# Kernel tuning notes

Measured on AMD Instinct MI355X. Metric: run time of the kernel, lower is better.

Reference implementation:

```python
import jax, jax.numpy as jnp
import numpy as np

B, V, M, L, D, OUT = 16, 16, 32, 24, 128, 193
VOCAB = {'cond': 5000, 'proc': 2000, 'drug': 600, 'lab_item': 700, 'lab_value': 200, 'inj_item': 400, 'inj_value': 200}


def setup_inputs() -> dict:
    key = jax.random.key(0)
    ks = iter(jax.random.split(key, 48))
    def emb_table(v):
        t = 0.02 * jax.random.normal(next(ks), (v, D), jnp.float32)
        return t.at[0].set(0.0)  # padding_idx = 0
    inp = {}
    inp['tok_cond'] = jax.random.randint(next(ks), (B, V, L), 0, VOCAB['cond'])
    inp['tok_proc'] = jax.random.randint(next(ks), (B, V, L), 0, VOCAB['proc'])
    inp['tok_drug'] = jax.random.randint(next(ks), (B, V, L), 0, VOCAB['drug'])
    inp['tok_lab_item'] = jax.random.randint(next(ks), (B, V, M, L), 0, VOCAB['lab_item'])
    inp['tok_lab_value'] = jax.random.randint(next(ks), (B, V, M, L), 0, VOCAB['lab_value'])
    inp['tok_inj_item'] = jax.random.randint(next(ks), (B, V, M, L), 0, VOCAB['inj_item'])
    inp['tok_inj_value'] = jax.random.randint(next(ks), (B, V, M, L), 0, VOCAB['inj_value'])
    inp['weight'] = jax.random.uniform(next(ks), (B, V, 1), jnp.float32)
    inp['age'] = jax.random.uniform(next(ks), (B, V, 1), jnp.float32)
    for n in ['cond', 'proc', 'drug', 'lab_item', 'lab_value', 'inj_item', 'inj_value']:
        inp['emb_' + n] = emb_table(VOCAB[n])
    def gru_params(nk):
        s = 0.05
        return (s * jax.random.normal(next(ks), (nk, 3 * D, D), jnp.float32),
                s * jax.random.normal(next(ks), (nk, 3 * D, D), jnp.float32),
                jnp.zeros((nk, 3 * D), jnp.float32),
                jnp.zeros((nk, 3 * D), jnp.float32))
    inp['mgru_wih'], inp['mgru_whh'], inp['mgru_bih'], inp['mgru_bhh'] = gru_params(5)
    inp['vgru_wih'], inp['vgru_whh'], inp['vgru_bih'], inp['vgru_bhh'] = gru_params(7)
    inp['info_w'] = 0.05 * jax.random.normal(next(ks), (2, D), jnp.float32)  # Linear(1, D) weights for weight/age
    inp['info_b'] = jnp.zeros((2, D), jnp.float32)
    inp['fc_w'] = 0.05 * jax.random.normal(next(ks), (7 * D, OUT), jnp.float32)
    inp['fc_b'] = jnp.zeros((OUT,), jnp.float32)
    return inp


def _gru(x, wih, whh, bih, bhh):
    # x: [N, T, Din]; torch nn.GRU semantics, gate order (r, z, n), h0 = 0
    n_, t_, _ = x.shape
    d = whh.shape[1]
    xg = jnp.einsum('ntd,gd->ntg', x, wih) + bih  # precompute input gates [N, T, 3D]
    def step(h, xg_t):
        gh = h @ whh.T + bhh
        ir, iz, inn = jnp.split(xg_t, 3, axis=-1)
        hr, hz, hn = jnp.split(gh, 3, axis=-1)
        r = jax.nn.sigmoid(ir + hr)
        z = jax.nn.sigmoid(iz + hz)
        n = jnp.tanh(inn + r * hn)
        h2 = (1.0 - z) * n + z * h
        return h2, h2
    h0 = jnp.zeros((n_, d), x.dtype)
    hT, outs = jax.lax.scan(step, h0, jnp.swapaxes(xg, 0, 1))
    return jnp.swapaxes(outs, 0, 1), hT  # output [N,T,D], hidden [N,D]

_gru_keys = jax.vmap(_gru)  # vmap over the per-feature-key leading axis


def reference(tok_cond, tok_proc, tok_drug, tok_lab_item, tok_lab_value, tok_inj_item, tok_inj_value,
              weight, age, emb_cond, emb_proc, emb_drug, emb_lab_item, emb_lab_value, emb_inj_item,
              emb_inj_value, mgru_wih, mgru_whh, mgru_bih, mgru_bhh, vgru_wih, vgru_whh, vgru_bih,
              vgru_bhh, info_w, info_b, fc_w, fc_b):
    b, v, m, _ = tok_lab_item.shape
    d = emb_cond.shape[1]
    # visit-event features: embedding + sum over code dim (dropout = identity, eval mode)
    e_cond = emb_cond[tok_cond].sum(axis=2)  # [B,V,D]
    e_proc = emb_proc[tok_proc].sum(axis=2)
    e_drug = emb_drug[tok_drug].sum(axis=2)
    # monitor-event pairs: elementwise mul of the two embeddings, sum over code dim
    lab = (emb_lab_item[tok_lab_item] * emb_lab_value[tok_lab_value]).sum(axis=3)  # [B,V,M,D]
    inj = (emb_inj_item[tok_inj_item] * emb_inj_value[tok_inj_value]).sum(axis=3)
    # repeat visit embeddings across the monitor axis (repeat(1, max_monitors, 1))
    rep = lambda e: jnp.broadcast_to(e[:, :, None, :], (b, v, m, d))
    mon_in = jnp.stack([rep(e_cond), rep(e_proc), rep(e_drug), lab, inj], axis=0)
    mon_in = mon_in.reshape(5, b * v, m, d)  # aggregate_tensors with uniform lengths
    # per-key monitor-level GRUs
    mon_out, mon_h = _gru_keys(mon_in, mgru_wih, mgru_whh, mgru_bih, mgru_bhh)
    # split_tensor + extract_and_transpose: take last monitor step per visit -> [5,B,V,D]
    last = mon_out[:, :, -1, :].reshape(5, b, v, d)
    # patient info Linear(1, D) for weight / age
    w_emb = weight * info_w[0] + info_b[0]  # [B,V,D]
    a_emb = age * info_w[1] + info_b[1]
    vis_in = jnp.concatenate([last, jnp.stack([w_emb, a_emb], axis=0)], axis=0)  # [7,B,V,D]
    # per-key visit-level GRUs
    _, vis_h = _gru_keys(vis_in, vgru_wih, vgru_whh, vgru_bih, vgru_bhh)  # [7,B,D]
    patient_emb = jnp.transpose(vis_h, (1, 0, 2)).reshape(b, 7 * d)  # concatenate_patient_embeddings
    logits = jax.nn.relu(patient_emb) @ fc_w + fc_b  # fc_patient: ReLU -> Linear(7D, output_size)
    return logits
```

## Files before the change

### kernel.cpp

```cpp
#include <hip/hip_runtime.h>
#include <stdint.h>

typedef unsigned short u16;
typedef unsigned int u32;

#define B_ 16
#define V_ 16
#define M_ 32
#define L_ 24
#define D_ 128
#define G_ 384
#define N_ 256
#define NM_ 8192
#define OUT_ 193

using bf16x8 = __attribute__((ext_vector_type(8))) __bf16;
using floatx4 = __attribute__((ext_vector_type(4))) float;

__device__ __forceinline__ float bf2f(u16 u) {
  u32 x = ((u32)u) << 16;
  return __builtin_bit_cast(float, x);
}
__device__ __forceinline__ u16 f2bf(float f) {
  u32 u = __builtin_bit_cast(u32, f);
  u = (u + 0x7FFFu + ((u >> 16) & 1u)) >> 16;
  return (u16)u;
}
__device__ __forceinline__ float sigm_(float x) {
  return __builtin_amdgcn_rcpf(1.0f + __expf(-x));
}
__device__ __forceinline__ float tanh_(float x) {
  float e = __expf(2.0f * x);
  return 1.0f - 2.0f * __builtin_amdgcn_rcpf(e + 1.0f);
}
__device__ __forceinline__ floatx4 mfma16(bf16x8 a, bf16x8 b, floatx4 c) {
  return __builtin_amdgcn_mfma_f32_16x16x32_bf16(a, b, c, 0, 0, 0);
}
__device__ __forceinline__ void lds_barrier() {
  asm volatile("s_waitcnt lgkmcnt(0)\n\ts_barrier" ::: "memory");
}

#define CONVB 4608
#define VEB 128
#define PEB 4096

__global__ __launch_bounds__(256) void k_stage1(
    const int* __restrict__ tc, const int* __restrict__ tp, const int* __restrict__ td,
    const int* __restrict__ tli, const int* __restrict__ tlv,
    const int* __restrict__ tii, const int* __restrict__ tiv,
    const float* __restrict__ ec, const float* __restrict__ ep, const float* __restrict__ ed,
    const float* __restrict__ eli, const float* __restrict__ elv,
    const float* __restrict__ eii, const float* __restrict__ eiv,
    const float* __restrict__ wv, const float* __restrict__ av,
    const float* __restrict__ iw, const float* __restrict__ ib,
    const float* __restrict__ mwih, const float* __restrict__ vwih,
    const float* __restrict__ mwhh, const float* __restrict__ vwhh,
    u16* __restrict__ wih_hi, u16* __restrict__ whh_hi,
    u16* __restrict__ ce_hi, u16* __restrict__ ce_lo,
    u16* __restrict__ vx_hi, u16* __restrict__ vx_lo,
    u16* __restrict__ mx_hi, u16* __restrict__ mx_lo) {
  int blk = blockIdx.x, tid = threadIdx.x;
  if (blk < CONVB) {
    const int SW = 12 * G_ * D_, S5 = 5 * G_ * D_;
    int i = blk * 256 + tid;
    if (i < SW) {
      float v = (i < S5) ? mwih[i] : vwih[i - S5];
      wih_hi[i] = f2bf(v);
    } else {
      int o = i - SW;
      float v = (o < S5) ? mwhh[o] : vwhh[o - S5];
      whh_hi[o] = f2bf(v);
    }
  } else if (blk < CONVB + VEB) {
    int n = (blk - CONVB) * 2 + (tid >> 7);
    int d = tid & 127;
    float a0 = 0.f, a1 = 0.f, a2 = 0.f;
#pragma unroll 4
    for (int l = 0; l < L_; l++) {
      a0 += ec[(size_t)tc[n * L_ + l] * D_ + d];
      a1 += ep[(size_t)tp[n * L_ + l] * D_ + d];
      a2 += ed[(size_t)td[n * L_ + l] * D_ + d];
    }
    size_t o0 = (size_t)n * D_ + d;
    u16 h;
    h = f2bf(a0); ce_hi[o0] = h;                   ce_lo[o0] = f2bf(a0 - bf2f(h));
    h = f2bf(a1); ce_hi[(size_t)N_ * D_ + o0] = h; ce_lo[(size_t)N_ * D_ + o0] = f2bf(a1 - bf2f(h));
    h = f2bf(a2); ce_hi[(size_t)2 * N_ * D_ + o0] = h; ce_lo[(size_t)2 * N_ * D_ + o0] = f2bf(a2 - bf2f(h));
    float wq = wv[n], aq = av[n];
    float v1 = wq * iw[d] + ib[d];
    float v2 = aq * iw[D_ + d] + ib[D_ + d];
    h = f2bf(v1); vx_hi[(size_t)5 * N_ * D_ + o0] = h; vx_lo[(size_t)5 * N_ * D_ + o0] = f2bf(v1 - bf2f(h));
    h = f2bf(v2); vx_hi[(size_t)6 * N_ * D_ + o0] = h; vx_lo[(size_t)6 * N_ * D_ + o0] = f2bf(v2 - bf2f(h));
  } else {
    int r = (blk - CONVB - VEB) * 2 + (tid >> 7);
    int d = tid & 127;
    float al = 0.f, ai = 0.f;
#pragma unroll 4
    for (int l = 0; l < L_; l++) {
      al += eli[(size_t)tli[r * L_ + l] * D_ + d] * elv[(size_t)tlv[r * L_ + l] * D_ + d];
      ai += eii[(size_t)tii[r * L_ + l] * D_ + d] * eiv[(size_t)tiv[r * L_ + l] * D_ + d];
    }
    size_t o = (size_t)r * D_ + d;
    u16 h;
    h = f2bf(al); mx_hi[o] = h;                    mx_lo[o] = f2bf(al - bf2f(h));
    h = f2bf(ai); mx_hi[(size_t)NM_ * D_ + o] = h; mx_lo[(size_t)NM_ * D_ + o] = f2bf(ai - bf2f(h));
  }
}

__global__ __launch_bounds__(256) void k_gemm_xg(
    const u16* __restrict__ A_hi, const u16* __restrict__ A_lo,
    const u16* __restrict__ W_hi,
    const float* __restrict__ bias,
    float* __restrict__ out, int A_ks, int W_ks, int b_ks, int o_ks) {
  int key = blockIdx.z;
  int w = threadIdx.x >> 6, lane = threadIdx.x & 63;
  int mq = lane & 15, q = lane >> 4;
  int row = blockIdx.x * 64 + w * 16;
  int cb = blockIdx.y * 96;

  const u16* Wk = W_hi + (size_t)key * W_ks;
  bf16x8 wf[6][4];
#pragma unroll
  for (int j = 0; j < 6; j++)
#pragma unroll
    for (int kk = 0; kk < 4; kk++)
      wf[j][kk] = *(const bf16x8*)(Wk + (size_t)(cb + j * 16 + mq) * D_ + kk * 32 + q * 8);

  const u16* Ah = A_hi + (size_t)key * A_ks + (size_t)(row + mq) * D_;
  const u16* Al = A_lo + (size_t)key * A_ks + (size_t)(row + mq) * D_;
  bf16x8 ah[4], al[4];
#pragma unroll
  for (int kk = 0; kk < 4; kk++) {
    ah[kk] = *(const bf16x8*)(Ah + kk * 32 + q * 8);
    al[kk] = *(const bf16x8*)(Al + kk * 32 + q * 8);
  }

  floatx4 acc[6];
#pragma unroll
  for (int j = 0; j < 6; j++) {
    float bv = bias[key * b_ks + cb + j * 16 + mq];
    acc[j] = {bv, bv, bv, bv};
  }
#pragma unroll
  for (int j = 0; j < 6; j++)
#pragma unroll
    for (int kk = 0; kk < 4; kk++) {
      acc[j] = mfma16(ah[kk], wf[j][kk], acc[j]);
      acc[j] = mfma16(al[kk], wf[j][kk], acc[j]);
    }

  float* op = out + (size_t)key * o_ks + (size_t)(row + q * 4) * G_ + cb + mq;
#pragma unroll
  for (int j = 0; j < 6; j++)
#pragma unroll
    for (int i = 0; i < 4; i++) op[(size_t)i * G_ + j * 16] = acc[j][i];
}

template <int MODE, int TT>
__global__ __launch_bounds__(512, 1) void k_gru8(
    int cpk, const float* __restrict__ xg_a, const float* __restrict__ xg_b,
    const u16* __restrict__ whh_all, const float* __restrict__ bhh_all,
    u16* __restrict__ out_hi, u16* __restrict__ out_lo, float* __restrict__ out_f32) {
  int key = blockIdx.x / cpk;
  int chunk = blockIdx.x % cpk;
  int n0 = chunk * 16;
  const u16* whh = whh_all + (size_t)key * (G_ * D_);
  const float* bhh = bhh_all + (size_t)key * G_;

  __shared__ u16 hls[2][2][16 * 128];

  int tid = threadIdx.x;
  int w = tid >> 6, lane = tid & 63, mq = lane & 15, q = lane >> 4;
  int dA = (w << 4) + mq;

  bf16x8 bw[3][4];
#pragma unroll
  for (int g = 0; g < 3; g++)
#pragma unroll
    for (int kk = 0; kk < 4; kk++)
      bw[g][kk] = *(const bf16x8*)(whh + (size_t)(g * 128 + dA) * D_ + kk * 32 + q * 8);

  floatx4 bseed[3];
#pragma unroll
  for (int g = 0; g < 3; g++) {
    float b = bhh[g * 128 + dA];
    bseed[g] = {b, b, b, b};
  }

  const float* xbase;
  size_t RS, TS;
  if (MODE == 0) {
    if (key < 3) { xbase = xg_a + ((size_t)key * N_ + n0) * G_; RS = G_; TS = 0; }
    else { xbase = xg_b + ((size_t)(key - 3) * NM_ + (size_t)n0 * M_) * G_; RS = (size_t)M_ * G_; TS = G_; }
  } else {
    xbase = xg_a + (size_t)key * N_ * G_; RS = (size_t)16 * G_; TS = G_;
  }
  const float* rowp[4];
#pragma unroll
  for (int i = 0; i < 4; i++) rowp[i] = xbase + (size_t)(q * 4 + i) * RS + dA;

  float xs[4][12];
#pragma unroll
  for (int s = 0; s < 3; s++) {
    int ts = s < TT ? s : TT - 1;
#pragma unroll
    for (int i = 0; i < 4; i++)
#pragma unroll
      for (int g = 0; g < 3; g++)
        xs[s][i * 3 + g] = rowp[i][(size_t)ts * TS + g * 128];
  }

  float h_old[4];
#pragma unroll
  for (int k = 0; k < 4; k++) h_old[k] = 0.f;

#define GRU_STEP(P)                                                                        \
  {                                                                                        \
    int t = tb + (P);                                                                      \
    {                                                                                      \
      int tpf = t + 3 < TT ? t + 3 : TT - 1;                                               \
      size_t to = (size_t)tpf * TS;                                                        \
      _Pragma("unroll") for (int i = 0; i < 4; i++)                                        \
          _Pragma("unroll") for (int g = 0; g < 3; g++)                                    \
              xs[((P) + 3) & 3][i * 3 + g] = rowp[i][to + g * 128];                        \
    }                                                                                      \
    floatx4 acc[3];                                                                        \
    if (t > 0) {                                                                           \
      const u16* hp0 = &hls[(t - 1) & 1][0][0];                                            \
      const u16* hp1 = &hls[(t - 1) & 1][1][0];                                            \
      bf16x8 ah[4], al[4];                                                                 \
      _Pragma("unroll") for (int kk = 0; kk < 4; kk++) {                                   \
        int off = mq * 128 + (((kk * 4 + q) ^ mq) * 8);                                    \
        ah[kk] = *(const bf16x8*)(hp0 + off);                                              \
        al[kk] = *(const bf16x8*)(hp1 + off);                                              \
      }                                                                                    \
      _Pragma("unroll") for (int g = 0; g < 3; g++) {                                      \
        floatx4 a = mfma16(ah[0], bw[g][0], bseed[g]);                                     \
        a = mfma16(al[0], bw[g][0], a);                                                    \
        a = mfma16(ah[1], bw[g][1], a);                                                    \
        a = mfma16(al[1], bw[g][1], a);                                                    \
        a = mfma16(ah[2], bw[g][2], a);                                                    \
        a = mfma16(al[2], bw[g][2], a);                                                    \
        a = mfma16(ah[3], bw[g][3], a);                                                    \
        acc[g] = mfma16(al[3], bw[g][3], a);                                               \
      }                                                                                    \
    } else {                                                                               \
      _Pragma("unroll") for (int g = 0; g < 3; g++) acc[g] = bseed[g];                     \
    }                                                                                      \
    u16* wrh = &hls[t & 1][0][0];                                                          \
    u16* wrl = &hls[t & 1][1][0];                                                          \
    _Pragma("unroll") for (int i = 0; i < 4; i++) {                                        \
      int row = q * 4 + i;                                                                 \
      float r = sigm_(xs[P][i * 3 + 0] + acc[0][i]);                                       \
      float z = sigm_(xs[P][i * 3 + 1] + acc[1][i]);                                       \
      float nn = tanh_(xs[P][i * 3 + 2] + r * acc[2][i]);                                  \
      float h2 = (1.0f - z) * nn + z * h_old[i];                                           \
      h_old[i] = h2;                                                                       \
      u32 ub = __builtin_bit_cast(u32, h2);                                                \
      u16 hb = (u16)(ub >> 16);                                                            \
      float rem = h2 - __builtin_bit_cast(float, ub & 0xFFFF0000u);                        \
      u16 lb = f2bf(rem);                                                                  \
      if (t == TT - 1) {                                                                   \
        if (MODE == 0) {                                                                   \
          size_t o = ((size_t)key * N_ + n0 + row) * D_ + dA;                              \
          out_hi[o] = hb;                                                                  \
          out_lo[o] = lb;                                                                  \
        } else {                                                                           \
          out_f32[((size_t)key * 16 + row) * D_ + dA] = h2;                                \
        }                                                                                  \
      } else {                                                                             \
        int idx = row * 128 + (((dA >> 3) ^ row) * 8) + (dA & 7);                          \
        wrh[idx] = hb;                                                                     \
        wrl[idx] = lb;                                                                     \
      }                                                                                    \
    }                                                                                      \
    if (t + 1 < TT) lds_barrier();                                                         \
  }

#pragma unroll 1
  for (int tb = 0; tb < TT; tb += 4) {
    GRU_STEP(0)
    GRU_STEP(1)
    GRU_STEP(2)
    GRU_STEP(3)
  }
#undef GRU_STEP
}

__global__ __launch_bounds__(256) void k_fc(
    const float* __restrict__ vis_h, const float* __restrict__ fc_w,
    const float* __restrict__ fc_b, float* __restrict__ out) {
  int b = blockIdx.x;
  int cg = blockIdx.y;
  int tid = threadIdx.x;
  int j = tid & 15, s = tid >> 4;
  int c = cg * 16 + j;
  bool cv = c < OUT_;

  __shared__ float hbuf[7 * D_];
  __shared__ float red[16][16];
  for (int i = tid; i < 7 * D_; i += 256) {
    float v = vis_h[((size_t)(i >> 7) * 16 + b) * D_ + (i & 127)];
    hbuf[i] = v > 0.f ? v : 0.f;
  }
  __syncthreads();

  float acc = 0.f;
  if (cv) {
    const float* wp = fc_w + (size_t)(s * 56) * OUT_ + c;
#pragma unroll 8
    for (int k = 0; k < 56; k++) acc += hbuf[s * 56 + k] * wp[(size_t)k * OUT_];
  }
  red[s][j] = acc;
  __syncthreads();
  if (s == 0 && cv) {
    float t = 0.f;
#pragma unroll
    for (int m = 0; m < 16; m++) t += red[m][j];
    out[(size_t)b * OUT_ + c] = t + fc_b[c];
  }
}

extern "C" void kernel_launch(void* const* d_in, const int* in_sizes, int n_in,
                              void* d_out, int out_size, void* d_ws, size_t ws_size,
                              hipStream_t stream) {
  (void)in_sizes; (void)n_in; (void)out_size; (void)ws_size;
  const int* tok_cond = (const int*)d_in[0];
  const int* tok_proc = (const int*)d_in[1];
  const int* tok_drug = (const int*)d_in[2];
  const int* tok_lab_item = (const int*)d_in[3];
  const int* tok_lab_value = (const int*)d_in[4];
  const int* tok_inj_item = (const int*)d_in[5];
  const int* tok_inj_value = (const int*)d_in[6];
  const float* weight = (const float*)d_in[7];
  const float* age = (const float*)d_in[8];
  const float* emb_cond = (const float*)d_in[9];
  const float* emb_proc = (const float*)d_in[10];
  const float* emb_drug = (const float*)d_in[11];
  const float* emb_lab_item = (const float*)d_in[12];
  const float* emb_lab_value = (const float*)d_in[13];
  const float* emb_inj_item = (const float*)d_in[14];
  const float* emb_inj_value = (const float*)d_in[15];
  const float* mgru_wih = (const float*)d_in[16];
  const float* mgru_whh = (const float*)d_in[17];
  const float* mgru_bih = (const float*)d_in[18];
  const float* mgru_bhh = (const float*)d_in[19];
  const float* vgru_wih = (const float*)d_in[20];
  const float* vgru_whh = (const float*)d_in[21];
  const float* vgru_bih = (const float*)d_in[22];
  const float* vgru_bhh = (const float*)d_in[23];
  const float* info_w = (const float*)d_in[24];
  const float* info_b = (const float*)d_in[25];
  const float* fc_w = (const float*)d_in[26];
  const float* fc_b = (const float*)d_in[27];

  char* p = (char*)d_ws;
  auto take = [&](size_t bytes) { char* r = p; p += (bytes + 255) & ~(size_t)255; return r; };
  u16* mx_hi = (u16*)take((size_t)2 * NM_ * D_ * 2);
  u16* mx_lo = (u16*)take((size_t)2 * NM_ * D_ * 2);
  u16* ce_hi = (u16*)take((size_t)3 * N_ * D_ * 2);
  u16* ce_lo = (u16*)take((size_t)3 * N_ * D_ * 2);
  u16* vx_hi = (u16*)take((size_t)7 * N_ * D_ * 2);
  u16* vx_lo = (u16*)take((size_t)7 * N_ * D_ * 2);
  float* xg_mon = (float*)take((size_t)2 * NM_ * G_ * 4);
  float* xg_c = (float*)take((size_t)3 * N_ * G_ * 4);
  float* xg_v = (float*)take((size_t)7 * N_ * G_ * 4);
  float* vis_h = (float*)take((size_t)7 * 16 * D_ * 4);
  u16* wih_hi = (u16*)take((size_t)12 * G_ * D_ * 2);
  u16* whh_hi = (u16*)take((size_t)12 * G_ * D_ * 2);

  k_stage1<<<CONVB + VEB + PEB, 256, 0, stream>>>(
      tok_cond, tok_proc, tok_drug, tok_lab_item, tok_lab_value, tok_inj_item, tok_inj_value,
      emb_cond, emb_proc, emb_drug, emb_lab_item, emb_lab_value, emb_inj_item, emb_inj_value,
      weight, age, info_w, info_b, mgru_wih, vgru_wih, mgru_whh, vgru_whh,
      wih_hi, whh_hi, ce_hi, ce_lo, vx_hi, vx_lo, mx_hi, mx_lo);
  k_gemm_xg<<<dim3(NM_ / 64, 4, 2), 256, 0, stream>>>(
      mx_hi, mx_lo, wih_hi + (size_t)3 * G_ * D_,
      mgru_bih + 3 * G_, xg_mon, NM_ * D_, G_ * D_, G_, NM_ * G_);
  k_gemm_xg<<<dim3(N_ / 64, 4, 3), 256, 0, stream>>>(
      ce_hi, ce_lo, wih_hi, mgru_bih, xg_c, N_ * D_, G_ * D_, G_, N_ * G_);
  k_gru8<0, 32><<<80, 512, 0, stream>>>(16, xg_c, xg_mon, whh_hi, mgru_bhh,
                                        vx_hi, vx_lo, nullptr);
  k_gemm_xg<<<dim3(N_ / 64, 4, 7), 256, 0, stream>>>(
      vx_hi, vx_lo, wih_hi + (size_t)5 * G_ * D_,
      vgru_bih, xg_v, N_ * D_, G_ * D_, G_, N_ * G_);
  k_gru8<1, 16><<<7, 512, 0, stream>>>(1, xg_v, nullptr, whh_hi + (size_t)5 * G_ * D_, vgru_bhh,
                                       nullptr, nullptr, vis_h);
  k_fc<<<dim3(B_, 13), 256, 0, stream>>>(vis_h, fc_w, fc_b, (float*)d_out);
}
```

Measured before the change: 222.0 us.

## Merge input-projection GEMMs into one launch and fuse visit GEMM into GRU

```diff
diff --git a/kernel.cpp b/kernel.cpp
--- a/kernel.cpp
+++ b/kernel.cpp
@@ -107,18 +107,40 @@
   }
 }
 
-__global__ __launch_bounds__(256) void k_gemm_xg(
-    const u16* __restrict__ A_hi, const u16* __restrict__ A_lo,
-    const u16* __restrict__ W_hi,
-    const float* __restrict__ bias,
-    float* __restrict__ out, int A_ks, int W_ks, int b_ks, int o_ks) {
-  int key = blockIdx.z;
+__global__ __launch_bounds__(256) void k_gemm_mon(
+    const u16* __restrict__ mx_hi, const u16* __restrict__ mx_lo,
+    const u16* __restrict__ ce_hi, const u16* __restrict__ ce_lo,
+    const u16* __restrict__ wih_hi, const float* __restrict__ mbih,
+    float* __restrict__ xg_mon, float* __restrict__ xg_c) {
+  int blk = blockIdx.x;
   int w = threadIdx.x >> 6, lane = threadIdx.x & 63;
   int mq = lane & 15, q = lane >> 4;
-  int row = blockIdx.x * 64 + w * 16;
-  int cb = blockIdx.y * 96;
-
-  const u16* Wk = W_hi + (size_t)key * W_ks;
+
+  const u16 *Ah, *Al, *Wk;
+  const float* bias;
+  float* out;
+  int row, cb;
+  if (blk < 1024) {
+    int key = blk >> 9, rem = blk & 511;
+    row = (rem >> 2) * 64 + w * 16;
+    cb = (blk & 3) * 96;
+    Ah = mx_hi + (size_t)key * NM_ * D_;
+    Al = mx_lo + (size_t)key * NM_ * D_;
+    Wk = wih_hi + (size_t)(3 + key) * G_ * D_;
+    bias = mbih + (3 + key) * G_;
+    out = xg_mon + (size_t)key * NM_ * G_;
+  } else {
+    int i = blk - 1024;
+    int key = i >> 4, rem = i & 15;
+    row = (rem >> 2) * 64 + w * 16;
+    cb = (i & 3) * 96;
+    Ah = ce_hi + (size_t)key * N_ * D_;
+    Al = ce_lo + (size_t)key * N_ * D_;
+    Wk = wih_hi + (size_t)key * G_ * D_;
+    bias = mbih + key * G_;
+    out = xg_c + (size_t)key * N_ * G_;
+  }
+
   bf16x8 wf[6][4];
 #pragma unroll
   for (int j = 0; j < 6; j++)
@@ -126,19 +148,19 @@
     for (int kk = 0; kk < 4; kk++)
       wf[j][kk] = *(const bf16x8*)(Wk + (size_t)(cb + j * 16 + mq) * D_ + kk * 32 + q * 8);
 
-  const u16* Ah = A_hi + (size_t)key * A_ks + (size_t)(row + mq) * D_;
-  const u16* Al = A_lo + (size_t)key * A_ks + (size_t)(row + mq) * D_;
+  const u16* Ar = Ah + (size_t)(row + mq) * D_;
+  const u16* Alr = Al + (size_t)(row + mq) * D_;
   bf16x8 ah[4], al[4];
 #pragma unroll
   for (int kk = 0; kk < 4; kk++) {
-    ah[kk] = *(const bf16x8*)(Ah + kk * 32 + q * 8);
-    al[kk] = *(const bf16x8*)(Al + kk * 32 + q * 8);
+    ah[kk] = *(const bf16x8*)(Ar + kk * 32 + q * 8);
+    al[kk] = *(const bf16x8*)(Alr + kk * 32 + q * 8);
   }
 
   floatx4 acc[6];
 #pragma unroll
   for (int j = 0; j < 6; j++) {
-    float bv = bias[key * b_ks + cb + j * 16 + mq];
+    float bv = bias[cb + j * 16 + mq];
     acc[j] = {bv, bv, bv, bv};
   }
 #pragma unroll
@@ -149,18 +171,18 @@
       acc[j] = mfma16(al[kk], wf[j][kk], acc[j]);
     }
 
-  float* op = out + (size_t)key * o_ks + (size_t)(row + q * 4) * G_ + cb + mq;
+  float* op = out + (size_t)(row + q * 4) * G_ + cb + mq;
 #pragma unroll
   for (int j = 0; j < 6; j++)
 #pragma unroll
     for (int i = 0; i < 4; i++) op[(size_t)i * G_ + j * 16] = acc[j][i];
 }
 
-template <int MODE, int TT>
+template <int TT>
 __global__ __launch_bounds__(512, 1) void k_gru8(
     int cpk, const float* __restrict__ xg_a, const float* __restrict__ xg_b,
     const u16* __restrict__ whh_all, const float* __restrict__ bhh_all,
-    u16* __restrict__ out_hi, u16* __restrict__ out_lo, float* __restrict__ out_f32) {
+    u16* __restrict__ out_hi, u16* __restrict__ out_lo) {
   int key = blockIdx.x / cpk;
   int chunk = blockIdx.x % cpk;
   int n0 = chunk * 16;
@@ -189,12 +211,8 @@
 
   const float* xbase;
   size_t RS, TS;
-  if (MODE == 0) {
-    if (key < 3) { xbase = xg_a + ((size_t)key * N_ + n0) * G_; RS = G_; TS = 0; }
-    else { xbase = xg_b + ((size_t)(key - 3) * NM_ + (size_t)n0 * M_) * G_; RS = (size_t)M_ * G_; TS = G_; }
-  } else {
-    xbase = xg_a + (size_t)key * N_ * G_; RS = (size_t)16 * G_; TS = G_;
-  }
+  if (key < 3) { xbase = xg_a + ((size_t)key * N_ + n0) * G_; RS = G_; TS = 0; }
+  else { xbase = xg_b + ((size_t)(key - 3) * NM_ + (size_t)n0 * M_) * G_; RS = (size_t)M_ * G_; TS = G_; }
   const float* rowp[4];
 #pragma unroll
   for (int i = 0; i < 4; i++) rowp[i] = xbase + (size_t)(q * 4 + i) * RS + dA;
@@ -261,13 +279,9 @@
       float rem = h2 - __builtin_bit_cast(float, ub & 0xFFFF0000u);                        \
       u16 lb = f2bf(rem);                                                                  \
       if (t == TT - 1) {                                                                   \
-        if (MODE == 0) {                                                                   \
-          size_t o = ((size_t)key * N_ + n0 + row) * D_ + dA;                              \
-          out_hi[o] = hb;                                                                  \
-          out_lo[o] = lb;                                                                  \
-        } else {                                                                           \
-          out_f32[((size_t)key * 16 + row) * D_ + dA] = h2;                                \
-        }                                                                                  \
+        size_t o = ((size_t)key * N_ + n0 + row) * D_ + dA;                                \
+        out_hi[o] = hb;                                                                    \
+        out_lo[o] = lb;                                                                    \
       } else {                                                                             \
         int idx = row * 128 + (((dA >> 3) ^ row) * 8) + (dA & 7);                          \
         wrh[idx] = hb;                                                                     \
@@ -285,6 +299,149 @@
     GRU_STEP(3)
   }
 #undef GRU_STEP
+}
+
+__global__ __launch_bounds__(512, 1) void k_gruv(
+    const u16* __restrict__ vx_hi, const u16* __restrict__ vx_lo,
+    const u16* __restrict__ wih_all, const u16* __restrict__ whh_all,
+    const float* __restrict__ bih_all, const float* __restrict__ bhh_all,
+    float* __restrict__ out_f32) {
+  const int TT = 16;
+  int key = blockIdx.x;
+  const u16* wih = wih_all + (size_t)key * (G_ * D_);
+  const u16* whh = whh_all + (size_t)key * (G_ * D_);
+  const float* bih = bih_all + (size_t)key * G_;
+  const float* bhh = bhh_all + (size_t)key * G_;
+
+  __shared__ u16 hls[2][2][16 * 128];
+
+  int tid = threadIdx.x;
+  int w = tid >> 6, lane = tid & 63, mq = lane & 15, q = lane >> 4;
+  int dA = (w << 4) + mq;
+  int ko = q * 8;
+
+  bf16x8 wf[3][4], bw[3][4];
+#pragma unroll
+  for (int g = 0; g < 3; g++)
+#pragma unroll
+    for (int kk = 0; kk < 4; kk++) {
+      size_t ro = (size_t)(g * 128 + dA) * D_ + kk * 32 + ko;
+      wf[g][kk] = *(const bf16x8*)(wih + ro);
+      bw[g][kk] = *(const bf16x8*)(whh + ro);
+    }
+
+  floatx4 bmerge[2], bxn, bhn;
+#pragma unroll
+  for (int g = 0; g < 2; g++) {
+    float b = bih[g * 128 + dA] + bhh[g * 128 + dA];
+    bmerge[g] = {b, b, b, b};
+  }
+  {
+    float bx = bih[2 * 128 + dA], bh = bhh[2 * 128 + dA];
+    bxn = {bx, bx, bx, bx};
+    bhn = {bh, bh, bh, bh};
+  }
+
+  const u16* tb_hi = vx_hi + ((size_t)key * N_ + mq * 16) * D_ + ko;
+  const u16* tb_lo = vx_lo + ((size_t)key * N_ + mq * 16) * D_ + ko;
+
+  bf16x8 xh[2][4], xl[2][4];
+#pragma unroll
+  for (int kk = 0; kk < 4; kk++) {
+    xh[0][kk] = *(const bf16x8*)(tb_hi + kk * 32);
+    xl[0][kk] = *(const bf16x8*)(tb_lo + kk * 32);
+    xh[1][kk] = *(const bf16x8*)(tb_hi + D_ + kk * 32);
+    xl[1][kk] = *(const bf16x8*)(tb_lo + D_ + kk * 32);
+  }
+
+  float h_old[4];
+#pragma unroll
+  for (int k = 0; k < 4; k++) h_old[k] = 0.f;
+
+#define GRUV_STEP(P)                                                                 \
+  {                                                                                  \
+    int t = tb + (P);                                                                \
+    floatx4 sm[2], sx, sh;                                                           \
+    _Pragma("unroll") for (int g = 0; g < 2; g++) {                                  \
+      floatx4 a = bmerge[g];                                                         \
+      _Pragma("unroll") for (int kk = 0; kk < 4; kk++) {                             \
+        a = mfma16(xh[P][kk], wf[g][kk], a);                                         \
+        a = mfma16(xl[P][kk], wf[g][kk], a);                                         \
+      }                                                                              \
+      sm[g] = a;                                                                     \
+    }                                                                                \
+    {                                                                                \
+      floatx4 a = bxn;                                                               \
+      _Pragma("unroll") for (int kk = 0; kk < 4; kk++) {                             \
+        a = mfma16(xh[P][kk], wf[2][kk], a);                                         \
+        a = mfma16(xl[P][kk], wf[2][kk], a);                                         \
+      }                                                                              \
+      sx = a;                                                                        \
+    }                                                                                \
+    sh = bhn;                                                                        \
+    if (t + 2 < TT) {                                                                \
+      size_t to = (size_t)(t + 2) * D_;                                              \
+      _Pragma("unroll") for (int kk = 0; kk < 4; kk++) {                             \
+        xh[P][kk] = *(const bf16x8*)(tb_hi + to + kk * 32);                          \
+        xl[P][kk] = *(const bf16x8*)(tb_lo + to + kk * 32);                          \
+      }                                                                              \
+    }                                                                                \
+    if (t > 0) {                                                                     \
+      const u16* hp0 = &hls[(t - 1) & 1][0][0];                                      \
+      const u16* hp1 = &hls[(t - 1) & 1][1][0];                                      \
+      bf16x8 ah[4], al[4];                                                           \
+      _Pragma("unroll") for (int kk = 0; kk < 4; kk++) {                             \
+        int off = mq * 128 + (((kk * 4 + q) ^ mq) * 8);                              \
+        ah[kk] = *(const bf16x8*)(hp0 + off);                                        \
+        al[kk] = *(const bf16x8*)(hp1 + off);                                        \
+      }                                                                              \
+      _Pragma("unroll") for (int g = 0; g < 2; g++) {                                \
+        floatx4 a = sm[g];                                                           \
+        _Pragma("unroll") for (int kk = 0; kk < 4; kk++) {                           \
+          a = mfma16(ah[kk], bw[g][kk], a);                                          \
+          a = mfma16(al[kk], bw[g][kk], a);                                          \
+        }                                                                            \
+        sm[g] = a;                                                                   \
+      }                                                                              \
+      {                                                                              \
+        floatx4 a = sh;                                                              \
+        _Pragma("unroll") for (int kk = 0; kk < 4; kk++) {                           \
+          a = mfma16(ah[kk], bw[2][kk], a);                                          \
+          a = mfma16(al[kk], bw[2][kk], a);                                          \
+        }                                                                            \
+        sh = a;                                                                      \
+      }                                                                              \
+    }                                                                                \
+    u16* wrh = &hls[t & 1][0][0];                                                    \
+    u16* wrl = &hls[t & 1][1][0];                                                    \
+    _Pragma("unroll") for (int i = 0; i < 4; i++) {                                  \
+      int row = q * 4 + i;                                                           \
+      float r = sigm_(sm[0][i]);                                                     \
+      float z = sigm_(sm[1][i]);                                                     \
+      float nn = tanh_(sx[i] + r * sh[i]);                                           \
+      float h2 = (1.0f - z) * nn + z * h_old[i];                                     \
+      h_old[i] = h2;                                                                 \
+      if (t == TT - 1) {                                                             \
+        out_f32[((size_t)key * 16 + row) * D_ + dA] = h2;                            \
+      } else {                                                                       \
+        u32 ub = __builtin_bit_cast(u32, h2);                                        \
+        u16 hb = (u16)(ub >> 16);                                                    \
+        float rem = h2 - __builtin_bit_cast(float, ub & 0xFFFF0000u);                \
+        u16 lb = f2bf(rem);                                                          \
+        int idx = row * 128 + (((dA >> 3) ^ row) * 8) + (dA & 7);                    \
+        wrh[idx] = hb;                                                               \
+        wrl[idx] = lb;                                                               \
+      }                                                                              \
+    }                                                                                \
+    if (t + 1 < TT) lds_barrier();                                                   \
+  }
+
+#pragma unroll 1
+  for (int tb = 0; tb < 16; tb += 2) {
+    GRUV_STEP(0)
+    GRUV_STEP(1)
+  }
+#undef GRUV_STEP
 }
 
 __global__ __launch_bounds__(256) void k_fc(
@@ -364,7 +521,6 @@
   u16* vx_lo = (u16*)take((size_t)7 * N_ * D_ * 2);
   float* xg_mon = (float*)take((size_t)2 * NM_ * G_ * 4);
   float* xg_c = (float*)take((size_t)3 * N_ * G_ * 4);
-  float* xg_v = (float*)take((size_t)7 * N_ * G_ * 4);
   float* vis_h = (float*)take((size_t)7 * 16 * D_ * 4);
   u16* wih_hi = (u16*)take((size_t)12 * G_ * D_ * 2);
   u16* whh_hi = (u16*)take((size_t)12 * G_ * D_ * 2);
@@ -374,17 +530,10 @@
       emb_cond, emb_proc, emb_drug, emb_lab_item, emb_lab_value, emb_inj_item, emb_inj_value,
       weight, age, info_w, info_b, mgru_wih, vgru_wih, mgru_whh, vgru_whh,
       wih_hi, whh_hi, ce_hi, ce_lo, vx_hi, vx_lo, mx_hi, mx_lo);
-  k_gemm_xg<<<dim3(NM_ / 64, 4, 2), 256, 0, stream>>>(
-      mx_hi, mx_lo, wih_hi + (size_t)3 * G_ * D_,
-      mgru_bih + 3 * G_, xg_mon, NM_ * D_, G_ * D_, G_, NM_ * G_);
-  k_gemm_xg<<<dim3(N_ / 64, 4, 3), 256, 0, stream>>>(
-      ce_hi, ce_lo, wih_hi, mgru_bih, xg_c, N_ * D_, G_ * D_, G_, N_ * G_);
-  k_gru8<0, 32><<<80, 512, 0, stream>>>(16, xg_c, xg_mon, whh_hi, mgru_bhh,
-                                        vx_hi, vx_lo, nullptr);
-  k_gemm_xg<<<dim3(N_ / 64, 4, 7), 256, 0, stream>>>(
-      vx_hi, vx_lo, wih_hi + (size_t)5 * G_ * D_,
-      vgru_bih, xg_v, N_ * D_, G_ * D_, G_, N_ * G_);
-  k_gru8<1, 16><<<7, 512, 0, stream>>>(1, xg_v, nullptr, whh_hi + (size_t)5 * G_ * D_, vgru_bhh,
-                                       nullptr, nullptr, vis_h);
+  k_gemm_mon<<<1072, 256, 0, stream>>>(mx_hi, mx_lo, ce_hi, ce_lo, wih_hi, mgru_bih,
+                                       xg_mon, xg_c);
+  k_gru8<32><<<80, 512, 0, stream>>>(16, xg_c, xg_mon, whh_hi, mgru_bhh, vx_hi, vx_lo);
+  k_gruv<<<7, 512, 0, stream>>>(vx_hi, vx_lo, wih_hi + (size_t)5 * G_ * D_,
+                                whh_hi + (size_t)5 * G_ * D_, vgru_bih, vgru_bhh, vis_h);
   k_fc<<<dim3(B_, 13), 256, 0, stream>>>(vis_h, fc_w, fc_b, (float*)d_out);
 }
```

After: 238.0 us. +7.2%, slower.
